# Optimization experiments

Measured on AMD Instinct MI355X. Metric: run time of the kernel, lower is better.

## Reference

```python
import jax, jax.numpy as jnp
import numpy as np

EPS = 1e-5

def _ln(x, g=None, b=None):
    m = jnp.mean(x, axis=-1, keepdims=True)
    v = jnp.var(x, axis=-1, keepdims=True)
    y = (x - m) / jnp.sqrt(v + EPS)
    if g is not None:
        y = y * g + b
    return y

def setup_inputs() -> dict:
    key = jax.random.key(0)
    B, N, C = 2, 2048, 1024   # batch, tokens, query_dim
    H, D = 16, 64             # heads, dim_head -> inner = 1024
    inner = H * D
    ks = jax.random.split(key, 8)
    s = C ** -0.5
    inp = {
        'x':   jax.random.normal(ks[0], (B, N, C), jnp.float32),
        'w_q': jax.random.normal(ks[1], (C, inner), jnp.float32) * s,
        'b_q': jnp.zeros((inner,), jnp.float32),
        'w_k': jax.random.normal(ks[2], (C, inner), jnp.float32) * s,
        'b_k': jnp.zeros((inner,), jnp.float32),
        'w_v': jax.random.normal(ks[3], (C, inner), jnp.float32) * s,
        'b_v': jnp.zeros((inner,), jnp.float32),
        'g_q': jnp.ones((inner,), jnp.float32),
        'be_q': jnp.zeros((inner,), jnp.float32),
        'g_k': jnp.ones((inner,), jnp.float32),
        'be_k': jnp.zeros((inner,), jnp.float32),
        # to_out is zero-initialized in the torch code; use small random weights
        # so forward/backward are non-trivial for correctness testing.
        'w_o': jax.random.normal(ks[4], (inner, C), jnp.float32) * s,
        'b_o': jnp.zeros((C,), jnp.float32),
    }
    return inp

def reference(x, w_q, b_q, w_k, b_k, w_v, b_v, g_q, be_q, g_k, be_k, w_o, b_o):
    B, N, C = x.shape
    inner = w_q.shape[1]
    H = 16
    D = inner // H
    xn = _ln(x)                                  # pre-norm, no affine
    ctx = xn                                     # self-attention (context=None)
    silu = jax.nn.silu
    q = silu(xn) @ w_q + b_q                     # [B,N,inner]
    k = silu(ctx) @ w_k + b_k
    v = silu(ctx) @ w_v + b_v
    q = _ln(q, g_q, be_q)
    k = _ln(k, g_k, be_k)
    q = q * (inner ** -0.5)                      # NB: scale by inner_dim, pre-split
    q = q.reshape(B, N, H, D)
    k = k.reshape(B, N, H, D)
    v = v.reshape(B, N, H, D)
    w = jnp.einsum('bihd,bjhd->bhij', q, k)      # [B,H,N,N]
    w = jax.nn.softmax(w, axis=-1)
    o = jnp.einsum('bhij,bjhd->bihd', w, v).reshape(B, N, inner)
    return silu(o) @ w_o + b_o
```

## Files before the change

### kernel.cpp

```cpp
#include <hip/hip_runtime.h>
#include <hip/hip_bf16.h>
#include <math.h>

#define LN_EPS 1e-5f

typedef __attribute__((ext_vector_type(8))) short bf16x8;
typedef __attribute__((ext_vector_type(4))) short bf16x4;
typedef __attribute__((ext_vector_type(8))) short short8;
typedef __attribute__((ext_vector_type(4))) float f32x4;
typedef unsigned short ushort_t;

__device__ __forceinline__ float silu_f(float x) {
    return x / (1.0f + __expf(-x));
}

__device__ __forceinline__ ushort_t f2bf(float f) {
    __hip_bfloat16 h = __float2bfloat16(f);
    return *reinterpret_cast<ushort_t*>(&h);
}

__device__ __forceinline__ float bf2f(ushort_t u) {
    __hip_bfloat16 h = *reinterpret_cast<__hip_bfloat16*>(&u);
    return __bfloat162float(h);
}

__device__ __forceinline__ unsigned pk2(float a, float b) {
#if defined(__has_builtin)
#if __has_builtin(__builtin_amdgcn_cvt_pk_bf16_f32)
    return __builtin_bit_cast(unsigned, __builtin_amdgcn_cvt_pk_bf16_f32(a, b));
#else
    return (((unsigned)f2bf(b)) << 16) | (unsigned)f2bf(a);
#endif
#else
    return (((unsigned)f2bf(b)) << 16) | (unsigned)f2bf(a);
#endif
}

__device__ __forceinline__ f32x4 mfma16(bf16x4 a, bf16x4 b, f32x4 c) {
#if defined(__has_builtin)
#if __has_builtin(__builtin_amdgcn_mfma_f32_16x16x16bf16_1k)
    return __builtin_amdgcn_mfma_f32_16x16x16bf16_1k(a, b, c, 0, 0, 0);
#elif __has_builtin(__builtin_amdgcn_mfma_f32_16x16x16_bf16)
    return __builtin_amdgcn_mfma_f32_16x16x16_bf16(a, b, c, 0, 0, 0);
#else
    f32x4 d = c;
    asm volatile("v_mfma_f32_16x16x16_bf16 %0, %1, %2, %0"
                 : "+v"(d) : "v"(a), "v"(b));
    return d;
#endif
#else
    f32x4 d = c;
    asm volatile("v_mfma_f32_16x16x16_bf16 %0, %1, %2, %0"
                 : "+v"(d) : "v"(a), "v"(b));
    return d;
#endif
}

__device__ __forceinline__ void gld16(const void* g, void* lds) {
    __builtin_amdgcn_global_load_lds(
        (const __attribute__((address_space(1))) unsigned int*)g,
        (__attribute__((address_space(3))) unsigned int*)lds, 16, 0, 0);
}

__device__ __forceinline__ float2 block_reduce2(float2 p, float2* sbuf) {
    #pragma unroll
    for (int off = 32; off > 0; off >>= 1) {
        p.x += __shfl_down(p.x, off, 64);
        p.y += __shfl_down(p.y, off, 64);
    }
    int lane = threadIdx.x & 63;
    int wid  = threadIdx.x >> 6;
    if (lane == 0) sbuf[wid] = p;
    __syncthreads();
    if (threadIdx.x == 0) {
        float2 r = sbuf[0];
        for (int i = 1; i < 4; ++i) { r.x += sbuf[i].x; r.y += sbuf[i].y; }
        sbuf[0] = r;
    }
    __syncthreads();
    return sbuf[0];
}

__global__ __launch_bounds__(256) void ln_silu_kernel(
    const float* __restrict__ x, ushort_t* __restrict__ out)
{
    __shared__ float2 sbuf[4];
    const int C = 1024;
    int row = blockIdx.x;
    const float4* xr = (const float4*)(x + (size_t)row * C);
    float4 v = xr[threadIdx.x];
    float2 p;
    p.x = v.x + v.y + v.z + v.w;
    p.y = v.x*v.x + v.y*v.y + v.z*v.z + v.w*v.w;
    float2 s = block_reduce2(p, sbuf);
    float mean = s.x / (float)C;
    float var  = s.y / (float)C - mean * mean;
    float rstd = rsqrtf(var + LN_EPS);
    ushort4 y;
    y.x = f2bf(silu_f((v.x - mean) * rstd));
    y.y = f2bf(silu_f((v.y - mean) * rstd));
    y.z = f2bf(silu_f((v.z - mean) * rstd));
    y.w = f2bf(silu_f((v.w - mean) * rstd));
    ((ushort4*)(out + (size_t)row * C))[threadIdx.x] = y;
}

__global__ __launch_bounds__(256) void ln_affine_bf16(
    ushort_t* __restrict__ q, const float* __restrict__ g,
    const float* __restrict__ be, float scale)
{
    __shared__ float2 sbuf[4];
    const int C = 1024;
    int row = blockIdx.x;
    ushort4 u = ((ushort4*)(q + (size_t)row * C))[threadIdx.x];
    float v0 = bf2f(u.x), v1 = bf2f(u.y), v2 = bf2f(u.z), v3 = bf2f(u.w);
    float2 p;
    p.x = v0 + v1 + v2 + v3;
    p.y = v0*v0 + v1*v1 + v2*v2 + v3*v3;
    float2 s = block_reduce2(p, sbuf);
    float mean = s.x / (float)C;
    float var  = s.y / (float)C - mean * mean;
    float rstd = rsqrtf(var + LN_EPS);
    float4 gv = ((const float4*)g)[threadIdx.x];
    float4 bv = ((const float4*)be)[threadIdx.x];
    ushort4 y;
    y.x = f2bf(((v0 - mean) * rstd * gv.x + bv.x) * scale);
    y.y = f2bf(((v1 - mean) * rstd * gv.y + bv.y) * scale);
    y.z = f2bf(((v2 - mean) * rstd * gv.z + bv.z) * scale);
    y.w = f2bf(((v3 - mean) * rstd * gv.w + bv.w) * scale);
    ((ushort4*)(q + (size_t)row * C))[threadIdx.x] = y;
}

struct W4 { const float* p[4]; };

__global__ __launch_bounds__(256) void transpose_w(W4 w, ushort_t* __restrict__ outbase)
{
    __shared__ float Ls[64][65];
    int z = blockIdx.z;
    const float* in = w.p[z];
    ushort_t* out = outbase + (size_t)z * 1024 * 1024;
    int r0 = blockIdx.y * 64, c0 = blockIdx.x * 64;
    int t = threadIdx.x, r = t >> 2, j = (t & 3) * 16;
    #pragma unroll
    for (int i = 0; i < 4; ++i) {
        float4 v = *(const float4*)(in + (size_t)(r0 + r) * 1024 + c0 + j + i * 4);
        Ls[r][j + i*4 + 0] = v.x;
        Ls[r][j + i*4 + 1] = v.y;
        Ls[r][j + i*4 + 2] = v.z;
        Ls[r][j + i*4 + 3] = v.w;
    }
    __syncthreads();
    __align__(16) ushort_t tmp[16];
    #pragma unroll
    for (int i = 0; i < 16; ++i) tmp[i] = f2bf(Ls[j + i][r]);
    ushort_t* op = out + (size_t)(c0 + r) * 1024 + r0 + j;
    *(short8*)(op)     = *(short8*)(tmp);
    *(short8*)(op + 8) = *(short8*)(tmp + 8);
}

template<int BM, bool OUT_BF16>
__global__ __launch_bounds__(256) void gemm_mfma(
    const ushort_t* __restrict__ A, const ushort_t* __restrict__ Bt0,
    const float* __restrict__ b0, const float* __restrict__ b1,
    const float* __restrict__ b2, void* __restrict__ out0,
    ushort_t* __restrict__ vt_out,
    int M, int N, int K)
{
    constexpr int BK = 64;
    constexpr int MI = BM / 32;
    __shared__ ushort_t As[BM * BK];
    __shared__ ushort_t Bs[128 * BK];

    int z = blockIdx.z;
    const ushort_t* Bt = Bt0 + (size_t)z * N * K;
    const float* bias = (z == 0) ? b0 : (z == 1) ? b1 : b2;

    int t = threadIdx.x;
    int lane = t & 63, wv = t >> 6;
    int wr = wv >> 1, wc = wv & 1;
    int quad = lane >> 4, ln16 = lane & 15;

    int row0 = blockIdx.y * BM;
    int col0 = blockIdx.x * 128;

    const f32x4 zero4 = {0.f, 0.f, 0.f, 0.f};
    f32x4 acc[MI][4];
    #pragma unroll
    for (int i = 0; i < MI; ++i)
        #pragma unroll
        for (int j = 0; j < 4; ++j) acc[i][j] = zero4;

    for (int kt = 0; kt < K; kt += BK) {
        #pragma unroll
        for (int c = 0; c < BM / 32; ++c) {
            int idx = c * 256 + t;
            int r = idx >> 3, ch = idx & 7;
            int g = ch ^ (r & 7);
            gld16(A + (size_t)(row0 + r) * K + kt + g * 8,
                  As + (size_t)(c * 256 + wv * 64) * 8);
        }
        #pragma unroll
        for (int c = 0; c < 4; ++c) {
            int idx = c * 256 + t;
            int r = idx >> 3, ch = idx & 7;
            int g = ch ^ (r & 7);
            gld16(Bt + (size_t)(col0 + r) * K + kt + g * 8,
                  Bs + (size_t)(c * 256 + wv * 64) * 8);
        }
        __syncthreads();
        #pragma unroll
        for (int s = 0; s < 2; ++s) {
            bf16x8 af[MI], bf[4];
            int g = s * 4 + quad;
            #pragma unroll
            for (int i = 0; i < MI; ++i) {
                int m = wr * (BM / 2) + i * 16 + ln16;
                af[i] = *(const bf16x8*)(As + (size_t)(m * 8 + (g ^ (m & 7))) * 8);
            }
            #pragma unroll
            for (int j = 0; j < 4; ++j) {
                int n = wc * 64 + j * 16 + ln16;
                bf[j] = *(const bf16x8*)(Bs + (size_t)(n * 8 + (g ^ (n & 7))) * 8);
            }
            #pragma unroll
            for (int i = 0; i < MI; ++i)
                #pragma unroll
                for (int j = 0; j < 4; ++j)
                    acc[i][j] = __builtin_amdgcn_mfma_f32_16x16x32_bf16(
                        af[i], bf[j], acc[i][j], 0, 0, 0);
        }
        __syncthreads();
    }

    if (OUT_BF16 && z == 2) {
        #pragma unroll
        for (int j = 0; j < 4; ++j) {
            int col = col0 + wc * 64 + j * 16 + ln16;
            float bv = bias[col];
            #pragma unroll
            for (int i = 0; i < MI; ++i) {
                int rowb = row0 + wr * (BM / 2) + i * 16 + quad * 4;
                int bb = rowb >> 11;
                int n0 = rowb & 2047;
                int pos = (n0 & ~31) | ((n0 & 12) << 1) | ((n0 & 16) >> 2);
                uint2 uu;
                uu.x = pk2(acc[i][j][0] + bv, acc[i][j][1] + bv);
                uu.y = pk2(acc[i][j][2] + bv, acc[i][j][3] + bv);
                *(uint2*)(vt_out + ((size_t)bb * 1024 + col) * 2048 + pos) = uu;
            }
        }
    } else {
        #pragma unroll
        for (int j = 0; j < 4; ++j) {
            int col = col0 + wc * 64 + j * 16 + ln16;
            float bv = bias[col];
            #pragma unroll
            for (int i = 0; i < MI; ++i) {
                int rowb = row0 + wr * (BM / 2) + i * 16 + quad * 4;
                #pragma unroll
                for (int r = 0; r < 4; ++r) {
                    float val = acc[i][j][r] + bv;
                    if (OUT_BF16) {
                        ushort_t* out = (ushort_t*)out0 + (size_t)z * M * N;
                        out[(size_t)(rowb + r) * N + col] = f2bf(val);
                    } else {
                        float* out = (float*)out0;
                        out[(size_t)(rowb + r) * N + col] = val;
                    }
                }
            }
        }
    }
}

__global__ __launch_bounds__(256, 4) void flash_mfma(
    const ushort_t* __restrict__ qb, const ushort_t* __restrict__ kb,
    const ushort_t* __restrict__ vT, ushort_t* __restrict__ ob)
{
    const int N = 2048, HD = 1024, D = 64, H = 16;
    const int KT = 128;
    __shared__ ushort_t Ks[128 * 64];
    __shared__ ushort_t Vs[64 * 128];

    int t = threadIdx.x, lane = t & 63, wv = t >> 6;
    int quad = lane >> 4, ln16 = lane & 15;
    int qt = blockIdx.x, h = blockIdx.y, b = blockIdx.z;

    size_t qk_base = (size_t)b * N * HD + (size_t)h * D;
    size_t vt_base = (size_t)(b * H + h) * D * N;

    bf16x8 qf[2];
    {
        const ushort_t* qp = qb + qk_base + (size_t)(qt * 64 + wv * 16 + ln16) * HD;
        qf[0] = *(const bf16x8*)(qp + quad * 8);
        qf[1] = *(const bf16x8*)(qp + 32 + quad * 8);
    }

    const f32x4 zero4 = {0.f, 0.f, 0.f, 0.f};
    f32x4 oacc[4];
    #pragma unroll
    for (int j = 0; j < 4; ++j) oacc[j] = zero4;
    float lcur = 0.f;

    for (int kt = 0; kt < N; kt += KT) {
        __syncthreads();
        #pragma unroll
        for (int c = 0; c < 4; ++c) {
            int idx = c * 256 + t;
            int r = idx >> 3, ch = idx & 7, g = ch ^ (r & 7);
            gld16(kb + qk_base + (size_t)(kt + r) * HD + g * 8,
                  Ks + (size_t)(c * 256 + wv * 64) * 8);
        }
        #pragma unroll
        for (int c = 0; c < 4; ++c) {
            int idx = c * 256 + t;
            int r = idx >> 4, ch = idx & 15, g = ch ^ (r & 15);
            gld16(vT + vt_base + (size_t)r * N + kt + g * 8,
                  Vs + (size_t)(c * 256 + wv * 64) * 8);
        }
        __syncthreads();

        f32x4 st[8];
        #pragma unroll
        for (int j = 0; j < 8; ++j) st[j] = zero4;
        #pragma unroll
        for (int s = 0; s < 2; ++s) {
            int g = s * 4 + quad;
            #pragma unroll
            for (int j = 0; j < 8; ++j) {
                int n = j * 16 + ln16;
                bf16x8 kf = *(const bf16x8*)(Ks + ((size_t)n * 8 + (g ^ (n & 7))) * 8);
                st[j] = __builtin_amdgcn_mfma_f32_16x16x32_bf16(kf, qf[s], st[j], 0, 0, 0);
            }
        }

        #pragma unroll
        for (int j = 0; j < 8; ++j) {
            st[j][0] = exp2f(st[j][0]);
            st[j][1] = exp2f(st[j][1]);
            st[j][2] = exp2f(st[j][2]);
            st[j][3] = exp2f(st[j][3]);
            lcur += (st[j][0] + st[j][1]) + (st[j][2] + st[j][3]);
        }

        #pragma unroll
        for (int w = 0; w < 4; ++w) {
            uint2 u0, u1;
            u0.x = pk2(st[2*w][0],   st[2*w][1]);
            u0.y = pk2(st[2*w][2],   st[2*w][3]);
            u1.x = pk2(st[2*w+1][0], st[2*w+1][1]);
            u1.y = pk2(st[2*w+1][2], st[2*w+1][3]);
            bf16x4 pf0 = __builtin_bit_cast(bf16x4, u0);
            bf16x4 pf1 = __builtin_bit_cast(bf16x4, u1);
            int lc = w * 4 + quad;
            #pragma unroll
            for (int mt = 0; mt < 4; ++mt) {
                int dd = mt * 16 + ln16;
                int phys = lc ^ ln16;
                bf16x8 vv = *(const bf16x8*)(Vs + (size_t)dd * 128 + phys * 8);
                bf16x4 vlo = __builtin_shufflevector(vv, vv, 0, 1, 2, 3);
                bf16x4 vhi = __builtin_shufflevector(vv, vv, 4, 5, 6, 7);
                oacc[mt] = mfma16(vlo, pf0, oacc[mt]);
                oacc[mt] = mfma16(vhi, pf1, oacc[mt]);
            }
        }
    }

    lcur += __shfl_xor(lcur, 16, 64);
    lcur += __shfl_xor(lcur, 32, 64);

    float inv = 1.0f / lcur;
    size_t rowoff = qk_base + (size_t)(qt * 64 + wv * 16 + ln16) * HD;
    #pragma unroll
    for (int mt = 0; mt < 4; ++mt) {
        float o0 = silu_f(oacc[mt][0] * inv);
        float o1 = silu_f(oacc[mt][1] * inv);
        float o2 = silu_f(oacc[mt][2] * inv);
        float o3 = silu_f(oacc[mt][3] * inv);
        uint2 uu;
        uu.x = pk2(o0, o1);
        uu.y = pk2(o2, o3);
        *(uint2*)(ob + rowoff + mt * 16 + quad * 4) = uu;
    }
}

extern "C" void kernel_launch(void* const* d_in, const int* in_sizes, int n_in,
                              void* d_out, int out_size, void* d_ws, size_t ws_size,
                              hipStream_t stream) {
    const float* x    = (const float*)d_in[0];
    const float* w_q  = (const float*)d_in[1];
    const float* b_q  = (const float*)d_in[2];
    const float* w_k  = (const float*)d_in[3];
    const float* b_k  = (const float*)d_in[4];
    const float* w_v  = (const float*)d_in[5];
    const float* b_v  = (const float*)d_in[6];
    const float* g_q  = (const float*)d_in[7];
    const float* be_q = (const float*)d_in[8];
    const float* g_k  = (const float*)d_in[9];
    const float* be_k = (const float*)d_in[10];
    const float* w_o  = (const float*)d_in[11];
    const float* b_o  = (const float*)d_in[12];
    float* out = (float*)d_out;

    const int B = 2, N = 2048, C = 1024, H = 16, INNER = 1024;
    const int M = B * N;
    const size_t MC = (size_t)M * C;

    ushort_t* ws  = (ushort_t*)d_ws;
    ushort_t* sx  = ws;
    ushort_t* qkv = ws + MC;
    ushort_t* vTp = ws + 4 * MC;
    ushort_t* wT  = ws + 5 * MC;

    ushort_t* qbuf = qkv;
    ushort_t* kbuf = qkv + MC;
    ushort_t* obuf = sx;

    W4 w4; w4.p[0] = w_q; w4.p[1] = w_k; w4.p[2] = w_v; w4.p[3] = w_o;
    transpose_w<<<dim3(16, 16, 4), 256, 0, stream>>>(w4, wT);

    ln_silu_kernel<<<M, 256, 0, stream>>>(x, sx);

    gemm_mfma<128, true><<<dim3(INNER / 128, M / 128, 3), 256, 0, stream>>>(
        sx, wT, b_q, b_k, b_v, qkv, vTp, M, INNER, C);

    ln_affine_bf16<<<M, 256, 0, stream>>>(qbuf, g_q, be_q, 0.03125f * 1.44269504f);
    ln_affine_bf16<<<M, 256, 0, stream>>>(kbuf, g_k, be_k, 1.0f);

    flash_mfma<<<dim3(N / 64, H, B), 256, 0, stream>>>(qbuf, kbuf, vTp, obuf);

    gemm_mfma<64, false><<<dim3(C / 128, M / 64, 1), 256, 0, stream>>>(
        obuf, wT + (size_t)3 * 1024 * 1024, b_o, b_o, b_o, out, nullptr, M, C, INNER);
}
```

Baseline: 242.7 us.

## Use 16x16x32 MFMA for PV, stage V-transpose through LDS, merge LN launches

In the attention kernel the P·V product now uses one 16x16x32 bf16 MFMA per tile instead of two 16x16x16 ones. K rows are loaded in a permuted order so the score layout matches the wider MFMA operand layout. The V-transpose epilogue of the QKV GEMM goes through swizzled shared memory, so it writes coalesced 16-byte rows instead of scattered 8-byte stores. The two LayerNorm launches for q and k are merged into one grid, and the reordering raises correctness risk if the permutations disagree.

After: 238.8 us. Within noise of the previous version (-1.6%).

```diff
diff --git a/kernel.cpp b/kernel.cpp
--- a/kernel.cpp
+++ b/kernel.cpp
@@ -5,7 +5,6 @@
 #define LN_EPS 1e-5f
 
 typedef __attribute__((ext_vector_type(8))) short bf16x8;
-typedef __attribute__((ext_vector_type(4))) short bf16x4;
 typedef __attribute__((ext_vector_type(8))) short short8;
 typedef __attribute__((ext_vector_type(4))) float f32x4;
 typedef unsigned short ushort_t;
@@ -33,26 +32,6 @@
 #endif
 #else
     return (((unsigned)f2bf(b)) << 16) | (unsigned)f2bf(a);
-#endif
-}
-
-__device__ __forceinline__ f32x4 mfma16(bf16x4 a, bf16x4 b, f32x4 c) {
-#if defined(__has_builtin)
-#if __has_builtin(__builtin_amdgcn_mfma_f32_16x16x16bf16_1k)
-    return __builtin_amdgcn_mfma_f32_16x16x16bf16_1k(a, b, c, 0, 0, 0);
-#elif __has_builtin(__builtin_amdgcn_mfma_f32_16x16x16_bf16)
-    return __builtin_amdgcn_mfma_f32_16x16x16_bf16(a, b, c, 0, 0, 0);
-#else
-    f32x4 d = c;
-    asm volatile("v_mfma_f32_16x16x16_bf16 %0, %1, %2, %0"
-                 : "+v"(d) : "v"(a), "v"(b));
-    return d;
-#endif
-#else
-    f32x4 d = c;
-    asm volatile("v_mfma_f32_16x16x16_bf16 %0, %1, %2, %0"
-                 : "+v"(d) : "v"(a), "v"(b));
-    return d;
 #endif
 }
 
@@ -105,11 +84,18 @@
 }
 
 __global__ __launch_bounds__(256) void ln_affine_bf16(
-    ushort_t* __restrict__ q, const float* __restrict__ g,
-    const float* __restrict__ be, float scale)
+    ushort_t* __restrict__ qk0, ushort_t* __restrict__ qk1,
+    const float* __restrict__ g0, const float* __restrict__ be0,
+    const float* __restrict__ g1, const float* __restrict__ be1,
+    float scale0, float scale1)
 {
     __shared__ float2 sbuf[4];
     const int C = 1024;
+    int which = blockIdx.y;
+    ushort_t* q = which ? qk1 : qk0;
+    const float* g  = which ? g1  : g0;
+    const float* be = which ? be1 : be0;
+    float scale = which ? scale1 : scale0;
     int row = blockIdx.x;
     ushort4 u = ((ushort4*)(q + (size_t)row * C))[threadIdx.x];
     float v0 = bf2f(u.x), v1 = bf2f(u.y), v2 = bf2f(u.z), v3 = bf2f(u.w);
@@ -167,8 +153,9 @@
 {
     constexpr int BK = 64;
     constexpr int MI = BM / 32;
-    __shared__ ushort_t As[BM * BK];
-    __shared__ ushort_t Bs[128 * BK];
+    __shared__ ushort_t Smem[(BM + 128) * BK];
+    ushort_t* As = Smem;
+    ushort_t* Bs = Smem + BM * BK;
 
     int z = blockIdx.z;
     const ushort_t* Bt = Bt0 + (size_t)z * N * K;
@@ -231,22 +218,33 @@
         __syncthreads();
     }
 
-    if (OUT_BF16 && z == 2) {
+    if (OUT_BF16 && z == 2 && BM == 128) {
+        ushort_t* tb = Smem + wv * 4096;
+        int tok0 = row0 + wr * 64;
+        int chn0 = col0 + wc * 64;
         #pragma unroll
         for (int j = 0; j < 4; ++j) {
-            int col = col0 + wc * 64 + j * 16 + ln16;
-            float bv = bias[col];
+            int chl = j * 16 + ln16;
+            float bv = bias[chn0 + chl];
             #pragma unroll
             for (int i = 0; i < MI; ++i) {
-                int rowb = row0 + wr * (BM / 2) + i * 16 + quad * 4;
-                int bb = rowb >> 11;
-                int n0 = rowb & 2047;
-                int pos = (n0 & ~31) | ((n0 & 12) << 1) | ((n0 & 16) >> 2);
                 uint2 uu;
                 uu.x = pk2(acc[i][j][0] + bv, acc[i][j][1] + bv);
                 uu.y = pk2(acc[i][j][2] + bv, acc[i][j][3] + bv);
-                *(uint2*)(vt_out + ((size_t)bb * 1024 + col) * 2048 + pos) = uu;
-            }
+                int hc = i * 4 + quad;
+                int phys = hc ^ ((chl & 7) << 1);
+                *(uint2*)(tb + chl * 64 + phys * 4) = uu;
+            }
+        }
+        int bb2 = tok0 >> 11;
+        int tokb = tok0 & 2047;
+        #pragma unroll
+        for (int p = 0; p < 8; ++p) {
+            int chl = p * 8 + (lane >> 3);
+            int tc  = lane & 7;
+            int ptc = tc ^ (chl & 7);
+            uint4 vvv = *(const uint4*)(tb + chl * 64 + ptc * 8);
+            *(uint4*)(vt_out + ((size_t)bb2 * 1024 + chn0 + chl) * 2048 + tokb + tc * 8) = vvv;
         }
     } else {
         #pragma unroll
@@ -307,7 +305,8 @@
         for (int c = 0; c < 4; ++c) {
             int idx = c * 256 + t;
             int r = idx >> 3, ch = idx & 7, g = ch ^ (r & 7);
-            gld16(kb + qk_base + (size_t)(kt + r) * HD + g * 8,
+            int pr = (r & ~31) | (((r >> 2) & 3) << 3) | (((r >> 4) & 1) << 2) | (r & 3);
+            gld16(kb + qk_base + (size_t)(kt + pr) * HD + g * 8,
                   Ks + (size_t)(c * 256 + wv * 64) * 8);
         }
         #pragma unroll
@@ -344,23 +343,19 @@
 
         #pragma unroll
         for (int w = 0; w < 4; ++w) {
-            uint2 u0, u1;
-            u0.x = pk2(st[2*w][0],   st[2*w][1]);
-            u0.y = pk2(st[2*w][2],   st[2*w][3]);
-            u1.x = pk2(st[2*w+1][0], st[2*w+1][1]);
-            u1.y = pk2(st[2*w+1][2], st[2*w+1][3]);
-            bf16x4 pf0 = __builtin_bit_cast(bf16x4, u0);
-            bf16x4 pf1 = __builtin_bit_cast(bf16x4, u1);
+            uint4 up;
+            up.x = pk2(st[2*w][0],   st[2*w][1]);
+            up.y = pk2(st[2*w][2],   st[2*w][3]);
+            up.z = pk2(st[2*w+1][0], st[2*w+1][1]);
+            up.w = pk2(st[2*w+1][2], st[2*w+1][3]);
+            bf16x8 pf = __builtin_bit_cast(bf16x8, up);
             int lc = w * 4 + quad;
             #pragma unroll
             for (int mt = 0; mt < 4; ++mt) {
                 int dd = mt * 16 + ln16;
                 int phys = lc ^ ln16;
-                bf16x8 vv = *(const bf16x8*)(Vs + (size_t)dd * 128 + phys * 8);
-                bf16x4 vlo = __builtin_shufflevector(vv, vv, 0, 1, 2, 3);
-                bf16x4 vhi = __builtin_shufflevector(vv, vv, 4, 5, 6, 7);
-                oacc[mt] = mfma16(vlo, pf0, oacc[mt]);
-                oacc[mt] = mfma16(vhi, pf1, oacc[mt]);
+                bf16x8 vf = *(const bf16x8*)(Vs + (size_t)dd * 128 + phys * 8);
+                oacc[mt] = __builtin_amdgcn_mfma_f32_16x16x32_bf16(vf, pf, oacc[mt], 0, 0, 0);
             }
         }
     }
@@ -423,8 +418,8 @@
     gemm_mfma<128, true><<<dim3(INNER / 128, M / 128, 3), 256, 0, stream>>>(
         sx, wT, b_q, b_k, b_v, qkv, vTp, M, INNER, C);
 
-    ln_affine_bf16<<<M, 256, 0, stream>>>(qbuf, g_q, be_q, 0.03125f * 1.44269504f);
-    ln_affine_bf16<<<M, 256, 0, stream>>>(kbuf, g_k, be_k, 1.0f);
+    ln_affine_bf16<<<dim3(M, 2), 256, 0, stream>>>(
+        qbuf, kbuf, g_q, be_q, g_k, be_k, 0.03125f * 1.44269504f, 1.0f);
 
     flash_mfma<<<dim3(N / 64, H, B), 256, 0, stream>>>(qbuf, kbuf, vTp, obuf);
 
```
